# Optimization experiments

Measured on AMD Instinct MI355X. Metric: run time of the kernel, lower is better.

## Reference

```python
import jax, jax.numpy as jnp
import numpy as np

D_IN = 1024
D_OUT = 1024
SEQ = 4096


def setup_inputs() -> dict:
    key = jax.random.key(0)
    kx, kq, kk, kv = jax.random.split(key, 4)
    s = 1.0 / np.sqrt(D_IN)
    return {
        "x": jax.random.normal(kx, (SEQ, D_IN), dtype=jnp.float32),
        # torch Linear weights: shape [d_out, d_in], y = x @ W.T
        "Wq": jax.random.uniform(kq, (D_OUT, D_IN), jnp.float32, -s, s),
        "Wk": jax.random.uniform(kk, (D_OUT, D_IN), jnp.float32, -s, s),
        "Wv": jax.random.uniform(kv, (D_OUT, D_IN), jnp.float32, -s, s),
    }


def reference(x, Wq, Wk, Wv):
    # QKV projections (no bias)
    q = x @ Wq.T  # [N, d_out]
    k = x @ Wk.T
    v = x @ Wv.T
    scale = 1.0 / jnp.sqrt(jnp.asarray(k.shape[-1], x.dtype))
    att = jax.nn.softmax((q @ k.T) * scale, axis=-1)  # [N, N]
    return att @ v  # [N, d_out]
```

## Files before the change

kernel.cpp:

```cpp
#include <hip/hip_runtime.h>
#include <hip/hip_bf16.h>
#include <math.h>

typedef __attribute__((ext_vector_type(8))) short short8;
typedef __attribute__((ext_vector_type(4))) float floatx4;

static __device__ __forceinline__ unsigned short f2bf(float f) {
    union { float f; unsigned int u; } a; a.f = f;
    unsigned int u = a.u;
    return (unsigned short)((u + 0x7FFFu + ((u >> 16) & 1u)) >> 16);
}

static __device__ __forceinline__ void cvt8(const float* __restrict__ src,
                                            unsigned short* __restrict__ dst, int i) {
    float4 v0 = *(const float4*)(src + i);
    float4 v1 = *(const float4*)(src + i + 4);
    ushort4 o0, o1;
    o0.x = f2bf(v0.x); o0.y = f2bf(v0.y); o0.z = f2bf(v0.z); o0.w = f2bf(v0.w);
    o1.x = f2bf(v1.x); o1.y = f2bf(v1.y); o1.z = f2bf(v1.z); o1.w = f2bf(v1.w);
    *(ushort4*)(dst + i) = o0;
    *(ushort4*)(dst + i + 4) = o1;
}

__global__ __launch_bounds__(256)
void cvt_x_zero(const float* __restrict__ src, unsigned short* __restrict__ dst,
                int n, float* __restrict__ l) {
    if ((int)blockIdx.x == gridDim.x - 1) {
        float4 z = {0.f, 0.f, 0.f, 0.f};
        #pragma unroll
        for (int c = 0; c < 4; c++)
            *(float4*)(l + threadIdx.x * 16 + c * 4) = z;
        return;
    }
    int i = (blockIdx.x * 256 + threadIdx.x) * 8;
    if (i < n) cvt8(src, dst, i);
}

struct W3 { const float* s[3]; unsigned short* d[3]; };
__global__ __launch_bounds__(256)
void cvt_w3(W3 a, int n) {
    int i = (blockIdx.x * 256 + threadIdx.x) * 8;
    if (i < n) cvt8(a.s[blockIdx.z], a.d[blockIdx.z], i);
}

template<int BM, int BN, int BK, int TI, int TJ, int WCOLS>
__device__ __forceinline__ void gemm_core(const unsigned short* __restrict__ A,
                                          const unsigned short* __restrict__ B,
                                          int lda, int k_begin, int k_end,
                                          unsigned short* sA, unsigned short* sB,
                                          floatx4 (&acc)[TI][TJ],
                                          int bm, int bn)
{
    constexpr int CPR = BK / 8;
    constexpr int RPR = 2048 / BK;
    const int t    = threadIdx.x;
    const int wave = t >> 6;
    const int lane = t & 63;
    const int wm = (wave / WCOLS) * (TI * 16);
    const int wn = (wave % WCOLS) * (TJ * 16);

    const int srow   = t / CPR;
    const int schunk = t % CPR;
    const int gchunk = schunk ^ (srow & (CPR - 1));
    const int lm  = lane & 15;
    const int swz = lm & (CPR - 1);

    for (int k0 = k_begin; k0 < k_end; k0 += BK) {
        __syncthreads();
        #pragma unroll
        for (int r = 0; r < (BM * BK) / 2048; r++) {
            const unsigned short* gA =
                A + (size_t)(bm + srow + r * RPR) * lda + k0 + gchunk * 8;
            __builtin_amdgcn_global_load_lds(
                (const __attribute__((address_space(1))) void*)gA,
                (__attribute__((address_space(3))) void*)((char*)sA + wave * 1024 + r * 4096),
                16, 0, 0);
        }
        #pragma unroll
        for (int r = 0; r < (BN * BK) / 2048; r++) {
            const unsigned short* gB =
                B + (size_t)(bn + srow + r * RPR) * lda + k0 + gchunk * 8;
            __builtin_amdgcn_global_load_lds(
                (const __attribute__((address_space(1))) void*)gB,
                (__attribute__((address_space(3))) void*)((char*)sB + wave * 1024 + r * 4096),
                16, 0, 0);
        }
        __syncthreads();

        #pragma unroll
        for (int kk = 0; kk < BK; kk += 32) {
            const int c  = (kk >> 3) + (lane >> 4);
            const int ce = ((c ^ swz) << 3);
            short8 a_frag[TI], b_frag[TJ];
            #pragma unroll
            for (int i = 0; i < TI; i++)
                a_frag[i] = *(const short8*)&sA[(wm + i * 16 + lm) * BK + ce];
            #pragma unroll
            for (int j = 0; j < TJ; j++)
                b_frag[j] = *(const short8*)&sB[(wn + j * 16 + lm) * BK + ce];
            #pragma unroll
            for (int i = 0; i < TI; i++)
                #pragma unroll
                for (int j = 0; j < TJ; j++)
                    acc[i][j] = __builtin_amdgcn_mfma_f32_16x16x32_bf16(
                        a_frag[i], b_frag[j], acc[i][j], 0, 0, 0);
        }
    }
}


struct P3 { const unsigned short* W[3]; unsigned short* O[3]; };
__global__ __launch_bounds__(256)
void proj3(const unsigned short* __restrict__ xb, P3 a) {
    __shared__ unsigned short sA[64 * 64];
    __shared__ unsigned short sB[128 * 64];
    const int z = blockIdx.z;
    const unsigned short* B = a.W[z];
    unsigned short* O = a.O[z];
    const bool trans = (z == 2);
    const int ldc = trans ? 4096 : 1024;
    const float scale = (z == 0) ? 0.03125f : 1.0f;

    floatx4 acc[4][2];
    #pragma unroll
    for (int i = 0; i < 4; i++)
        #pragma unroll
        for (int j = 0; j < 2; j++) { floatx4 zz = {0.f,0.f,0.f,0.f}; acc[i][j] = zz; }

    const int bm = blockIdx.y * 64, bn = blockIdx.x * 128;
    gemm_core<64, 128, 64, 4, 2, 4>(xb, B, 1024, 0, 1024, sA, sB, acc, bm, bn);

    const int lane = threadIdx.x & 63, wave = threadIdx.x >> 6;
    const int wn = (wave & 3) * 32;
    const int lm = lane & 15, rq = (lane >> 4) * 4;
    #pragma unroll
    for (int i = 0; i < 4; i++)
        #pragma unroll
        for (int j = 0; j < 2; j++) {
            int tm = bm + i * 16 + rq;
            int tn = bn + wn + j * 16 + lm;
            #pragma unroll
            for (int r = 0; r < 4; r++) {
                unsigned short h = f2bf(acc[i][j][r] * scale);
                size_t idx = trans ? ((size_t)tn * ldc + (tm + r))
                                   : ((size_t)(tm + r) * ldc + tn);
                O[idx] = h;
            }
        }
}

__global__ __launch_bounds__(256)
void gemm_ps(const unsigned short* __restrict__ q, const unsigned short* __restrict__ k,
             unsigned short* __restrict__ Pm, float* __restrict__ l) {
    __shared__ unsigned short sA[128 * 128];
    __shared__ unsigned short sB[128 * 128];

    floatx4 acc[4][4];
    #pragma unroll
    for (int i = 0; i < 4; i++)
        #pragma unroll
        for (int j = 0; j < 4; j++) { floatx4 zz = {0.f,0.f,0.f,0.f}; acc[i][j] = zz; }

    const int bm = blockIdx.y * 128, bn = blockIdx.x * 128;
    gemm_core<128, 128, 128, 4, 4, 2>(q, k, 1024, 0, 1024, sA, sB, acc, bm, bn);

    const int lane = threadIdx.x & 63, wave = threadIdx.x >> 6;
    const int wm = (wave >> 1) * 64, wn = (wave & 1) * 64;
    const int lm = lane & 15, rq = (lane >> 4) * 4;
    #pragma unroll
    for (int i = 0; i < 4; i++) {
        #pragma unroll
        for (int r = 0; r < 4; r++) {
            int row = bm + wm + i * 16 + rq + r;
            float rs = 0.f;
            #pragma unroll
            for (int j = 0; j < 4; j++) {
                float e = __expf(acc[i][j][r]);
                rs += e;
                int tn = bn + wn + j * 16 + lm;
                Pm[(size_t)row * 4096 + tn] = f2bf(e);
            }
            rs += __shfl_xor(rs, 1);
            rs += __shfl_xor(rs, 2);
            rs += __shfl_xor(rs, 4);
            rs += __shfl_xor(rs, 8);
            if (lm == 0) atomicAdd(l + row, rs);
        }
    }
}

__global__ __launch_bounds__(256)
void gemm_osplit(const unsigned short* __restrict__ Pm, const unsigned short* __restrict__ vT,
                 float* __restrict__ Opart) {
    __shared__ unsigned short sA[64 * 128];
    __shared__ unsigned short sB[128 * 128];

    floatx4 acc[4][2];
    #pragma unroll
    for (int i = 0; i < 4; i++)
        #pragma unroll
        for (int j = 0; j < 2; j++) { floatx4 zz = {0.f,0.f,0.f,0.f}; acc[i][j] = zz; }

    const int z = blockIdx.z;
    const int bm = blockIdx.y * 64, bn = blockIdx.x * 128;
    gemm_core<64, 128, 128, 4, 2, 4>(Pm, vT, 4096, z * 2048, (z + 1) * 2048,
                                     sA, sB, acc, bm, bn);

    float* Op = Opart + (size_t)z * (4096 * 1024);
    const int lane = threadIdx.x & 63, wave = threadIdx.x >> 6;
    const int wn = (wave & 3) * 32;
    const int lm = lane & 15, rq = (lane >> 4) * 4;
    #pragma unroll
    for (int i = 0; i < 4; i++)
        #pragma unroll
        for (int j = 0; j < 2; j++) {
            int tm = bm + i * 16 + rq;
            int tn = bn + wn + j * 16 + lm;
            #pragma unroll
            for (int r = 0; r < 4; r++)
                Op[(size_t)(tm + r) * 1024 + tn] = acc[i][j][r];
        }
}

__global__ __launch_bounds__(256)
void reduce_scale(const float* __restrict__ Op, const float* __restrict__ l,
                  float* __restrict__ out) {
    int i = (blockIdx.x * 256 + threadIdx.x) * 4;
    float4 a = *(const float4*)(Op + i);
    float4 b = *(const float4*)(Op + 4096 * 1024 + i);
    float inv = 1.0f / l[i >> 10];
    float4 o;
    o.x = (a.x + b.x) * inv; o.y = (a.y + b.y) * inv;
    o.z = (a.z + b.z) * inv; o.w = (a.w + b.w) * inv;
    *(float4*)(out + i) = o;
}

extern "C" void kernel_launch(void* const* d_in, const int* in_sizes, int n_in,
                              void* d_out, int out_size, void* d_ws, size_t ws_size,
                              hipStream_t stream) {
    const float* x  = (const float*)d_in[0];
    const float* Wq = (const float*)d_in[1];
    const float* Wk = (const float*)d_in[2];
    const float* Wv = (const float*)d_in[3];
    float* out = (float*)d_out;

    const int SEQ = 4096, D = 1024;
    char* ws = (char*)d_ws;
    const size_t MB = 1u << 20;
    unsigned short* vTb = (unsigned short*)(ws);
    unsigned short* xb  = (unsigned short*)(ws + 8 * MB);
    unsigned short* Wqb = (unsigned short*)(ws + 16 * MB);
    unsigned short* Wkb = (unsigned short*)(ws + 18 * MB);
    unsigned short* Wvb = (unsigned short*)(ws + 20 * MB);
    unsigned short* qb  = (unsigned short*)(ws + 22 * MB);
    unsigned short* kb  = (unsigned short*)(ws + 30 * MB);
    unsigned short* P   = (unsigned short*)(ws + 38 * MB);
    float*          l   = (float*)(ws + 70 * MB);
    float*          Opart = (float*)(ws + 72 * MB);

    dim3 blk(256);
    cvt_x_zero<<<(SEQ * D) / 2048 + 1, blk, 0, stream>>>(x, xb, SEQ * D, l);
    W3 w3 = {{Wq, Wk, Wv}, {Wqb, Wkb, Wvb}};
    cvt_w3<<<dim3((D * D) / 2048, 1, 3), blk, 0, stream>>>(w3, D * D);

    P3 p3 = {{Wqb, Wkb, Wvb}, {qb, kb, vTb}};
    proj3<<<dim3(D / 128, SEQ / 64, 3), blk, 0, stream>>>(xb, p3);

    gemm_ps<<<dim3(SEQ / 128, SEQ / 128), blk, 0, stream>>>(qb, kb, P, l);

    gemm_osplit<<<dim3(D / 128, SEQ / 64, 2), blk, 0, stream>>>(P, vTb, Opart);

    reduce_scale<<<(SEQ * D) / 1024, blk, 0, stream>>>(Opart, l, out);
}
```

Measured before the change: 236.3 us.

## Merge conversion kernels, enlarge GEMM tiles, and remap blocks for XCD locality

The three conversion launches are merged into one kernel that converts x, converts the weights and zeroes the row-sum buffer. The projection and PV GEMMs move from 64x128 to 128x128 tiles, which raises reuse per block but halves the number of blocks. The QK^T and PV kernels now use a 1D grid with an explicit mapping meant to group blocks that share operands on the same XCD for L2 reuse. Larger tiles increase register and LDS use and may lower occupancy.

After: 219.3 us. 7.2% less time.

```diff
diff --git a/kernel.cpp b/kernel.cpp
--- a/kernel.cpp
+++ b/kernel.cpp
@@ -22,25 +22,23 @@
     *(ushort4*)(dst + i + 4) = o1;
 }
 
-__global__ __launch_bounds__(256)
-void cvt_x_zero(const float* __restrict__ src, unsigned short* __restrict__ dst,
-                int n, float* __restrict__ l) {
-    if ((int)blockIdx.x == gridDim.x - 1) {
-        float4 z = {0.f, 0.f, 0.f, 0.f};
+struct CV { const float* x; unsigned short* xb;
+            const float* W[3]; unsigned short* Wb[3]; float* l; };
+__global__ __launch_bounds__(256)
+void cvt_all(CV a) {
+    int b = blockIdx.x, t = threadIdx.x;
+    if (b < 2048) {
+        cvt8(a.x, a.xb, (b * 256 + t) * 8);
+    } else if (b < 3584) {
+        int z  = (b - 2048) >> 9;
+        int bb = (b - 2048) & 511;
+        cvt8(a.W[z], a.Wb[z], (bb * 256 + t) * 8);
+    } else {
+        float4 zz = {0.f, 0.f, 0.f, 0.f};
         #pragma unroll
         for (int c = 0; c < 4; c++)
-            *(float4*)(l + threadIdx.x * 16 + c * 4) = z;
-        return;
+            *(float4*)(a.l + t * 16 + c * 4) = zz;
     }
-    int i = (blockIdx.x * 256 + threadIdx.x) * 8;
-    if (i < n) cvt8(src, dst, i);
-}
-
-struct W3 { const float* s[3]; unsigned short* d[3]; };
-__global__ __launch_bounds__(256)
-void cvt_w3(W3 a, int n) {
-    int i = (blockIdx.x * 256 + threadIdx.x) * 8;
-    if (i < n) cvt8(a.s[blockIdx.z], a.d[blockIdx.z], i);
 }
 
 template<int BM, int BN, int BK, int TI, int TJ, int WCOLS>
@@ -112,7 +110,7 @@
 struct P3 { const unsigned short* W[3]; unsigned short* O[3]; };
 __global__ __launch_bounds__(256)
 void proj3(const unsigned short* __restrict__ xb, P3 a) {
-    __shared__ unsigned short sA[64 * 64];
+    __shared__ unsigned short sA[128 * 64];
     __shared__ unsigned short sB[128 * 64];
     const int z = blockIdx.z;
     const unsigned short* B = a.W[z];
@@ -121,23 +119,23 @@
     const int ldc = trans ? 4096 : 1024;
     const float scale = (z == 0) ? 0.03125f : 1.0f;
 
-    floatx4 acc[4][2];
-    #pragma unroll
-    for (int i = 0; i < 4; i++)
-        #pragma unroll
-        for (int j = 0; j < 2; j++) { floatx4 zz = {0.f,0.f,0.f,0.f}; acc[i][j] = zz; }
-
-    const int bm = blockIdx.y * 64, bn = blockIdx.x * 128;
-    gemm_core<64, 128, 64, 4, 2, 4>(xb, B, 1024, 0, 1024, sA, sB, acc, bm, bn);
+    floatx4 acc[4][4];
+    #pragma unroll
+    for (int i = 0; i < 4; i++)
+        #pragma unroll
+        for (int j = 0; j < 4; j++) { floatx4 zz = {0.f,0.f,0.f,0.f}; acc[i][j] = zz; }
+
+    const int bm = blockIdx.y * 128, bn = blockIdx.x * 128;
+    gemm_core<128, 128, 64, 4, 4, 2>(xb, B, 1024, 0, 1024, sA, sB, acc, bm, bn);
 
     const int lane = threadIdx.x & 63, wave = threadIdx.x >> 6;
-    const int wn = (wave & 3) * 32;
+    const int wm = (wave >> 1) * 64, wn = (wave & 1) * 64;
     const int lm = lane & 15, rq = (lane >> 4) * 4;
     #pragma unroll
     for (int i = 0; i < 4; i++)
         #pragma unroll
-        for (int j = 0; j < 2; j++) {
-            int tm = bm + i * 16 + rq;
+        for (int j = 0; j < 4; j++) {
+            int tm = bm + wm + i * 16 + rq;
             int tn = bn + wn + j * 16 + lm;
             #pragma unroll
             for (int r = 0; r < 4; r++) {
@@ -155,13 +153,19 @@
     __shared__ unsigned short sA[128 * 128];
     __shared__ unsigned short sB[128 * 128];
 
+    const int lid = blockIdx.x;
+    const int xcd = lid & 7;
+    const int i8  = lid >> 3;
+    const int by  = (xcd & 1) * 16 + (i8 & 15);
+    const int bx  = (xcd >> 1) * 8 + (i8 >> 4);
+
     floatx4 acc[4][4];
     #pragma unroll
     for (int i = 0; i < 4; i++)
         #pragma unroll
         for (int j = 0; j < 4; j++) { floatx4 zz = {0.f,0.f,0.f,0.f}; acc[i][j] = zz; }
 
-    const int bm = blockIdx.y * 128, bn = blockIdx.x * 128;
+    const int bm = by * 128, bn = bx * 128;
     gemm_core<128, 128, 128, 4, 4, 2>(q, k, 1024, 0, 1024, sA, sB, acc, bm, bn);
 
     const int lane = threadIdx.x & 63, wave = threadIdx.x >> 6;
@@ -192,29 +196,36 @@
 __global__ __launch_bounds__(256)
 void gemm_osplit(const unsigned short* __restrict__ Pm, const unsigned short* __restrict__ vT,
                  float* __restrict__ Opart) {
-    __shared__ unsigned short sA[64 * 128];
+    __shared__ unsigned short sA[128 * 128];
     __shared__ unsigned short sB[128 * 128];
 
-    floatx4 acc[4][2];
-    #pragma unroll
-    for (int i = 0; i < 4; i++)
-        #pragma unroll
-        for (int j = 0; j < 2; j++) { floatx4 zz = {0.f,0.f,0.f,0.f}; acc[i][j] = zz; }
-
-    const int z = blockIdx.z;
-    const int bm = blockIdx.y * 64, bn = blockIdx.x * 128;
-    gemm_core<64, 128, 128, 4, 2, 4>(Pm, vT, 4096, z * 2048, (z + 1) * 2048,
-                                     sA, sB, acc, bm, bn);
+    const int lid = blockIdx.x;
+    const int xcd = lid & 7;
+    const int w   = lid >> 6;
+    const int g   = (lid >> 3) & 7;
+    const int s   = w * 8 + xcd;
+    const int z   = s >> 5;
+    const int row = s & 31;
+
+    floatx4 acc[4][4];
+    #pragma unroll
+    for (int i = 0; i < 4; i++)
+        #pragma unroll
+        for (int j = 0; j < 4; j++) { floatx4 zz = {0.f,0.f,0.f,0.f}; acc[i][j] = zz; }
+
+    const int bm = row * 128, bn = g * 128;
+    gemm_core<128, 128, 128, 4, 4, 2>(Pm, vT, 4096, z * 2048, (z + 1) * 2048,
+                                      sA, sB, acc, bm, bn);
 
     float* Op = Opart + (size_t)z * (4096 * 1024);
     const int lane = threadIdx.x & 63, wave = threadIdx.x >> 6;
-    const int wn = (wave & 3) * 32;
+    const int wm = (wave >> 1) * 64, wn = (wave & 1) * 64;
     const int lm = lane & 15, rq = (lane >> 4) * 4;
     #pragma unroll
     for (int i = 0; i < 4; i++)
         #pragma unroll
-        for (int j = 0; j < 2; j++) {
-            int tm = bm + i * 16 + rq;
+        for (int j = 0; j < 4; j++) {
+            int tm = bm + wm + i * 16 + rq;
             int tn = bn + wn + j * 16 + lm;
             #pragma unroll
             for (int r = 0; r < 4; r++)
@@ -259,16 +270,15 @@
     float*          Opart = (float*)(ws + 72 * MB);
 
     dim3 blk(256);
-    cvt_x_zero<<<(SEQ * D) / 2048 + 1, blk, 0, stream>>>(x, xb, SEQ * D, l);
-    W3 w3 = {{Wq, Wk, Wv}, {Wqb, Wkb, Wvb}};
-    cvt_w3<<<dim3((D * D) / 2048, 1, 3), blk, 0, stream>>>(w3, D * D);
+    CV cv = {x, xb, {Wq, Wk, Wv}, {Wqb, Wkb, Wvb}, l};
+    cvt_all<<<dim3(3585), blk, 0, stream>>>(cv);
 
     P3 p3 = {{Wqb, Wkb, Wvb}, {qb, kb, vTb}};
-    proj3<<<dim3(D / 128, SEQ / 64, 3), blk, 0, stream>>>(xb, p3);
-
-    gemm_ps<<<dim3(SEQ / 128, SEQ / 128), blk, 0, stream>>>(qb, kb, P, l);
-
-    gemm_osplit<<<dim3(D / 128, SEQ / 64, 2), blk, 0, stream>>>(P, vTb, Opart);
+    proj3<<<dim3(D / 128, SEQ / 128, 3), blk, 0, stream>>>(xb, p3);
+
+    gemm_ps<<<dim3(1024), blk, 0, stream>>>(qb, kb, P, l);
+
+    gemm_osplit<<<dim3(512), blk, 0, stream>>>(P, vTb, Opart);
 
     reduce_scale<<<(SEQ * D) / 1024, blk, 0, stream>>>(Opart, l, out);
 }
```
